# Kernel optimization log

Hardware: AMD Instinct MI355X
Metric: run time of the kernel (lower is better)

## Reference

```python
import jax, jax.numpy as jnp
import numpy as np

HIDDEN = 32
INPUT = 1
OUTPUT = 1


def setup_inputs() -> dict:
    key = jax.random.key(0)
    ks = jax.random.split(key, 7)
    B, T = 4096, 512
    s_ih = 1.0 / np.sqrt(HIDDEN)
    x = jax.random.normal(ks[0], (B, T, INPUT), dtype=jnp.float32)
    # PyTorch LSTM params, gate order i, f, g, o
    W_ih = jax.random.uniform(ks[1], (4 * HIDDEN, INPUT), jnp.float32, -s_ih, s_ih)
    W_hh = jax.random.uniform(ks[2], (4 * HIDDEN, HIDDEN), jnp.float32, -s_ih, s_ih)
    b_ih = jax.random.uniform(ks[3], (4 * HIDDEN,), jnp.float32, -s_ih, s_ih)
    b_hh = jax.random.uniform(ks[4], (4 * HIDDEN,), jnp.float32, -s_ih, s_ih)
    W_fc = jax.random.uniform(ks[5], (OUTPUT, HIDDEN), jnp.float32, -s_ih, s_ih)
    b_fc = jax.random.uniform(ks[6], (OUTPUT,), jnp.float32, -s_ih, s_ih)
    return {"x": x, "W_ih": W_ih, "W_hh": W_hh, "b_ih": b_ih,
            "b_hh": b_hh, "W_fc": W_fc, "b_fc": b_fc}


def _lstm_last_h(x, W_ih, W_hh, b_ih, b_hh):
    B = x.shape[0]
    H = W_hh.shape[1]
    # precompute input contribution for all timesteps: [T, B, 4H]
    xg = jnp.einsum('bti,gi->tbg', x, W_ih) + (b_ih + b_hh)

    def step(carry, xg_t):
        h, c = carry
        gates = xg_t + h @ W_hh.T  # [B, 4H]
        i, f, g, o = jnp.split(gates, 4, axis=-1)
        i = jax.nn.sigmoid(i)
        f = jax.nn.sigmoid(f)
        g = jnp.tanh(g)
        o = jax.nn.sigmoid(o)
        c = f * c + i * g
        h = o * jnp.tanh(c)
        return (h, c), None

    h0 = jnp.zeros((B, H), x.dtype)
    c0 = jnp.zeros((B, H), x.dtype)
    (hT, _), _ = jax.lax.scan(step, (h0, c0), xg)
    return hT  # last timestep hidden state [B, H]


def reference(x, W_ih, W_hh, b_ih, b_hh, W_fc, b_fc):
    hT = _lstm_last_h(x, W_ih, W_hh, b_ih, b_hh)
    return hT @ W_fc.T + b_fc  # [B, OUTPUT]
```

## Files before the change

kernel.cpp:

```cpp
#include <hip/hip_runtime.h>


#define HID 32
#define TSTEPS 512
#define BPW 2
#define BLOCK 64

__device__ __forceinline__ float rcp_fast(float x) {
    return __builtin_amdgcn_rcpf(x);
}
__device__ __forceinline__ float sigmoid_fast(float x) {
    return rcp_fast(1.0f + __expf(-x));
}
__device__ __forceinline__ float tanh_fast(float x) {
    return fmaf(2.0f, rcp_fast(1.0f + __expf(-2.0f * x)), -1.0f);
}

__global__ __launch_bounds__(BLOCK)
__attribute__((amdgpu_waves_per_eu(2, 2)))
void lstm_fused_kernel(const float* __restrict__ x,
                       const float* __restrict__ W_ih,
                       const float* __restrict__ W_hh,
                       const float* __restrict__ b_ih,
                       const float* __restrict__ b_hh,
                       const float* __restrict__ W_fc,
                       const float* __restrict__ b_fc,
                       float* __restrict__ out)
{
    __shared__ __align__(16) float x_s[BPW * TSTEPS];
    __shared__ __align__(16) float h_s[BPW][HID];

    const int tid = threadIdx.x;
    const int lb  = tid >> 5;
    const int j   = tid & 31;
    const int b0  = blockIdx.x * BPW;

    {
        const float4* xsrc = reinterpret_cast<const float4*>(x + (size_t)b0 * TSTEPS);
        float4* xdst = reinterpret_cast<float4*>(x_s);
        #pragma unroll
        for (int k = 0; k < (BPW * TSTEPS) / (4 * BLOCK); ++k)
            xdst[tid + k * BLOCK] = xsrc[tid + k * BLOCK];
    }

    float w0[HID], w1[HID], w2[HID], w3[HID];
    {
        const float4* r0 = reinterpret_cast<const float4*>(W_hh + (size_t)(0 * HID + j) * HID);
        const float4* r1 = reinterpret_cast<const float4*>(W_hh + (size_t)(1 * HID + j) * HID);
        const float4* r2 = reinterpret_cast<const float4*>(W_hh + (size_t)(2 * HID + j) * HID);
        const float4* r3 = reinterpret_cast<const float4*>(W_hh + (size_t)(3 * HID + j) * HID);
        #pragma unroll
        for (int k = 0; k < HID / 4; ++k) {
            float4 v;
            v = r0[k]; w0[4*k]=v.x; w0[4*k+1]=v.y; w0[4*k+2]=v.z; w0[4*k+3]=v.w;
            v = r1[k]; w1[4*k]=v.x; w1[4*k+1]=v.y; w1[4*k+2]=v.z; w1[4*k+3]=v.w;
            v = r2[k]; w2[4*k]=v.x; w2[4*k+1]=v.y; w2[4*k+2]=v.z; w2[4*k+3]=v.w;
            v = r3[k]; w3[4*k]=v.x; w3[4*k+1]=v.y; w3[4*k+2]=v.z; w3[4*k+3]=v.w;
        }
    }
    const float wih0 = W_ih[j],           wih1 = W_ih[HID + j];
    const float wih2 = W_ih[2*HID + j],   wih3 = W_ih[3*HID + j];
    const float bs0  = b_ih[j]           + b_hh[j];
    const float bs1  = b_ih[HID + j]     + b_hh[HID + j];
    const float bs2  = b_ih[2*HID + j]   + b_hh[2*HID + j];
    const float bs3  = b_ih[3*HID + j]   + b_hh[3*HID + j];

    h_s[lb][j] = 0.0f;
    float c = 0.0f;
    float hcur = 0.0f;
    __syncthreads();

    #pragma unroll 1
    for (int t = 0; t < TSTEPS; ++t) {
        const float xv = x_s[lb * TSTEPS + t];

        float a0 = fmaf(xv, wih0, bs0);
        float a1 = fmaf(xv, wih1, bs1);
        float a2 = fmaf(xv, wih2, bs2);
        float a3 = fmaf(xv, wih3, bs3);

        const float4* hr = reinterpret_cast<const float4*>(&h_s[lb][0]);
        #pragma unroll
        for (int k = 0; k < HID / 4; ++k) {
            float4 hv = hr[k];
            a0 = fmaf(hv.x, w0[4*k  ], a0);
            a1 = fmaf(hv.x, w1[4*k  ], a1);
            a2 = fmaf(hv.x, w2[4*k  ], a2);
            a3 = fmaf(hv.x, w3[4*k  ], a3);
            a0 = fmaf(hv.y, w0[4*k+1], a0);
            a1 = fmaf(hv.y, w1[4*k+1], a1);
            a2 = fmaf(hv.y, w2[4*k+1], a2);
            a3 = fmaf(hv.y, w3[4*k+1], a3);
            a0 = fmaf(hv.z, w0[4*k+2], a0);
            a1 = fmaf(hv.z, w1[4*k+2], a1);
            a2 = fmaf(hv.z, w2[4*k+2], a2);
            a3 = fmaf(hv.z, w3[4*k+2], a3);
            a0 = fmaf(hv.w, w0[4*k+3], a0);
            a1 = fmaf(hv.w, w1[4*k+3], a1);
            a2 = fmaf(hv.w, w2[4*k+3], a2);
            a3 = fmaf(hv.w, w3[4*k+3], a3);
        }

        const float ig = sigmoid_fast(a0);
        const float fg = sigmoid_fast(a1);
        const float gg = tanh_fast(a2);
        const float og = sigmoid_fast(a3);
        c    = fmaf(fg, c, ig * gg);
        hcur = og * tanh_fast(c);

        h_s[lb][j] = hcur;
        asm volatile("" ::: "memory");
    }

    float p = hcur * W_fc[j];
    #pragma unroll
    for (int off = 16; off >= 1; off >>= 1)
        p += __shfl_xor(p, off);
    if (j == 0)
        out[b0 + lb] = p + b_fc[0];
}

extern "C" void kernel_launch(void* const* d_in, const int* in_sizes, int n_in,
                              void* d_out, int out_size, void* d_ws, size_t ws_size,
                              hipStream_t stream) {
    const float* x    = (const float*)d_in[0];
    const float* W_ih = (const float*)d_in[1];
    const float* W_hh = (const float*)d_in[2];
    const float* b_ih = (const float*)d_in[3];
    const float* b_hh = (const float*)d_in[4];
    const float* W_fc = (const float*)d_in[5];
    const float* b_fc = (const float*)d_in[6];
    float* out = (float*)d_out;

    const int B = in_sizes[0] / TSTEPS;
    const int grid = B / BPW;
    lstm_fused_kernel<<<grid, BLOCK, 0, stream>>>(x, W_ih, W_hh, b_ih, b_hh,
                                                  W_fc, b_fc, out);
}
```

Measured before the change: 277.1 us.

## Use packed FP32 FMA for recurrent matvec and fold log2e into weights

Stores the W_hh rows as float2 pairs and replaces the scalar FMA chain with v_pk_fma_f32, splitting each gate accumulator into two lanes that are summed at the end. The log2(e) factor, and 2·log2(e) for the tanh gate, is folded into the recurrent weights, input weights and biases, so the activations can call exp2 directly without a multiply. The waves_per_eu attribute is replaced by launch_bounds(64,2). Packed FMA halves the VALU instruction count of the inner product and shortens each serial accumulation chain. The exchange is an extra horizontal add per gate, possible register or packing overhead, and slightly different rounding.

Result: slower. 305.1 us (+10.1%).

```diff
diff --git a/kernel.cpp b/kernel.cpp
--- a/kernel.cpp
+++ b/kernel.cpp
@@ -5,19 +5,27 @@
 #define TSTEPS 512
 #define BPW 2
 #define BLOCK 64
+#define L2E 1.44269504088896340736f
 
+__device__ __forceinline__ float2 pk_fma(float2 a, float2 b, float2 c) {
+    float2 d;
+    asm("v_pk_fma_f32 %0, %1, %2, %3" : "=v"(d) : "v"(a), "v"(b), "v"(c));
+    return d;
+}
 __device__ __forceinline__ float rcp_fast(float x) {
     return __builtin_amdgcn_rcpf(x);
 }
-__device__ __forceinline__ float sigmoid_fast(float x) {
-    return rcp_fast(1.0f + __expf(-x));
+__device__ __forceinline__ float exp2_fast(float x) {
+    return __builtin_amdgcn_exp2f(x);
 }
-__device__ __forceinline__ float tanh_fast(float x) {
-    return fmaf(2.0f, rcp_fast(1.0f + __expf(-2.0f * x)), -1.0f);
+__device__ __forceinline__ float sigmoid_l2(float a) {
+    return rcp_fast(1.0f + exp2_fast(-a));
+}
+__device__ __forceinline__ float tanh_l2(float a) {
+    return fmaf(2.0f, rcp_fast(1.0f + exp2_fast(-a)), -1.0f);
 }
 
-__global__ __launch_bounds__(BLOCK)
-__attribute__((amdgpu_waves_per_eu(2, 2)))
+__global__ __launch_bounds__(BLOCK, 2)
 void lstm_fused_kernel(const float* __restrict__ x,
                        const float* __restrict__ W_ih,
                        const float* __restrict__ W_hh,
@@ -43,7 +51,7 @@
             xdst[tid + k * BLOCK] = xsrc[tid + k * BLOCK];
     }
 
-    float w0[HID], w1[HID], w2[HID], w3[HID];
+    float2 w0[HID/2], w1[HID/2], w2[HID/2], w3[HID/2];
     {
         const float4* r0 = reinterpret_cast<const float4*>(W_hh + (size_t)(0 * HID + j) * HID);
         const float4* r1 = reinterpret_cast<const float4*>(W_hh + (size_t)(1 * HID + j) * HID);
@@ -52,18 +60,24 @@
         #pragma unroll
         for (int k = 0; k < HID / 4; ++k) {
             float4 v;
-            v = r0[k]; w0[4*k]=v.x; w0[4*k+1]=v.y; w0[4*k+2]=v.z; w0[4*k+3]=v.w;
-            v = r1[k]; w1[4*k]=v.x; w1[4*k+1]=v.y; w1[4*k+2]=v.z; w1[4*k+3]=v.w;
-            v = r2[k]; w2[4*k]=v.x; w2[4*k+1]=v.y; w2[4*k+2]=v.z; w2[4*k+3]=v.w;
-            v = r3[k]; w3[4*k]=v.x; w3[4*k+1]=v.y; w3[4*k+2]=v.z; w3[4*k+3]=v.w;
+            v = r0[k]; w0[2*k] = make_float2(v.x*L2E, v.y*L2E);
+                       w0[2*k+1] = make_float2(v.z*L2E, v.w*L2E);
+            v = r1[k]; w1[2*k] = make_float2(v.x*L2E, v.y*L2E);
+                       w1[2*k+1] = make_float2(v.z*L2E, v.w*L2E);
+            v = r2[k]; w2[2*k] = make_float2(v.x*2.0f*L2E, v.y*2.0f*L2E);
+                       w2[2*k+1] = make_float2(v.z*2.0f*L2E, v.w*2.0f*L2E);
+            v = r3[k]; w3[2*k] = make_float2(v.x*L2E, v.y*L2E);
+                       w3[2*k+1] = make_float2(v.z*L2E, v.w*L2E);
         }
     }
-    const float wih0 = W_ih[j],           wih1 = W_ih[HID + j];
-    const float wih2 = W_ih[2*HID + j],   wih3 = W_ih[3*HID + j];
-    const float bs0  = b_ih[j]           + b_hh[j];
-    const float bs1  = b_ih[HID + j]     + b_hh[HID + j];
-    const float bs2  = b_ih[2*HID + j]   + b_hh[2*HID + j];
-    const float bs3  = b_ih[3*HID + j]   + b_hh[3*HID + j];
+    const float wih0 = W_ih[j]         * L2E;
+    const float wih1 = W_ih[HID + j]   * L2E;
+    const float wih2 = W_ih[2*HID + j] * 2.0f * L2E;
+    const float wih3 = W_ih[3*HID + j] * L2E;
+    const float bs0  = (b_ih[j]         + b_hh[j])         * L2E;
+    const float bs1  = (b_ih[HID + j]   + b_hh[HID + j])   * L2E;
+    const float bs2  = (b_ih[2*HID + j] + b_hh[2*HID + j]) * 2.0f * L2E;
+    const float bs3  = (b_ih[3*HID + j] + b_hh[3*HID + j]) * L2E;
 
     h_s[lb][j] = 0.0f;
     float c = 0.0f;
@@ -74,39 +88,37 @@
     for (int t = 0; t < TSTEPS; ++t) {
         const float xv = x_s[lb * TSTEPS + t];
 
-        float a0 = fmaf(xv, wih0, bs0);
-        float a1 = fmaf(xv, wih1, bs1);
-        float a2 = fmaf(xv, wih2, bs2);
-        float a3 = fmaf(xv, wih3, bs3);
+        float2 acc0 = make_float2(fmaf(xv, wih0, bs0), 0.0f);
+        float2 acc1 = make_float2(fmaf(xv, wih1, bs1), 0.0f);
+        float2 acc2 = make_float2(fmaf(xv, wih2, bs2), 0.0f);
+        float2 acc3 = make_float2(fmaf(xv, wih3, bs3), 0.0f);
 
         const float4* hr = reinterpret_cast<const float4*>(&h_s[lb][0]);
         #pragma unroll
         for (int k = 0; k < HID / 4; ++k) {
             float4 hv = hr[k];
-            a0 = fmaf(hv.x, w0[4*k  ], a0);
-            a1 = fmaf(hv.x, w1[4*k  ], a1);
-            a2 = fmaf(hv.x, w2[4*k  ], a2);
-            a3 = fmaf(hv.x, w3[4*k  ], a3);
-            a0 = fmaf(hv.y, w0[4*k+1], a0);
-            a1 = fmaf(hv.y, w1[4*k+1], a1);
-            a2 = fmaf(hv.y, w2[4*k+1], a2);
-            a3 = fmaf(hv.y, w3[4*k+1], a3);
-            a0 = fmaf(hv.z, w0[4*k+2], a0);
-            a1 = fmaf(hv.z, w1[4*k+2], a1);
-            a2 = fmaf(hv.z, w2[4*k+2], a2);
-            a3 = fmaf(hv.z, w3[4*k+2], a3);
-            a0 = fmaf(hv.w, w0[4*k+3], a0);
-            a1 = fmaf(hv.w, w1[4*k+3], a1);
-            a2 = fmaf(hv.w, w2[4*k+3], a2);
-            a3 = fmaf(hv.w, w3[4*k+3], a3);
+            float2 hA = make_float2(hv.x, hv.y);
+            float2 hB = make_float2(hv.z, hv.w);
+            acc0 = pk_fma(hA, w0[2*k], acc0);
+            acc1 = pk_fma(hA, w1[2*k], acc1);
+            acc2 = pk_fma(hA, w2[2*k], acc2);
+            acc3 = pk_fma(hA, w3[2*k], acc3);
+            acc0 = pk_fma(hB, w0[2*k+1], acc0);
+            acc1 = pk_fma(hB, w1[2*k+1], acc1);
+            acc2 = pk_fma(hB, w2[2*k+1], acc2);
+            acc3 = pk_fma(hB, w3[2*k+1], acc3);
         }
+        const float a0 = acc0.x + acc0.y;
+        const float a1 = acc1.x + acc1.y;
+        const float a2 = acc2.x + acc2.y;
+        const float a3 = acc3.x + acc3.y;
 
-        const float ig = sigmoid_fast(a0);
-        const float fg = sigmoid_fast(a1);
-        const float gg = tanh_fast(a2);
-        const float og = sigmoid_fast(a3);
+        const float ig = sigmoid_l2(a0);
+        const float fg = sigmoid_l2(a1);
+        const float gg = tanh_l2(a2);
+        const float og = sigmoid_l2(a3);
         c    = fmaf(fg, c, ig * gg);
-        hcur = og * tanh_fast(c);
+        hcur = og * tanh_l2((2.0f * L2E) * c);
 
         h_s[lb][j] = hcur;
         asm volatile("" ::: "memory");
```

## Hand-write the LSTM recurrence loop in inline GCN assembly

Applied to the files above, without the earlier changes.

Replaces the compiler-generated time loop with a single inline-asm block. W_hh rows are held in fixed VGPRs, h is read from LDS with b128 reads and waitcnt is placed by hand, followed by 128 v_fmac ops and an explicit exp/rcp gate sequence. The aim is to avoid compiler spills and poor scheduling with 128 live weights and to shorten the per-step serial chain. It hardcodes register numbers and relies on wave lockstep for LDS ordering with no barrier, so correctness and portability are fragile.

After: 277.6 us. About the same (+0.2%).

```diff
diff --git a/kernel.cpp b/kernel.cpp
--- a/kernel.cpp
+++ b/kernel.cpp
@@ -1,4 +1,5 @@
 #include <hip/hip_runtime.h>
+#include <stdint.h>
 
 
 #define HID 32
@@ -6,15 +7,11 @@
 #define BPW 2
 #define BLOCK 64
 
-__device__ __forceinline__ float rcp_fast(float x) {
-    return __builtin_amdgcn_rcpf(x);
-}
-__device__ __forceinline__ float sigmoid_fast(float x) {
-    return rcp_fast(1.0f + __expf(-x));
-}
-__device__ __forceinline__ float tanh_fast(float x) {
-    return fmaf(2.0f, rcp_fast(1.0f + __expf(-2.0f * x)), -1.0f);
-}
+#define FMA4(h,wi,wf,wg,wo) \
+  "v_fmac_f32 v192, v" h ", v" wi "\n\t" \
+  "v_fmac_f32 v193, v" h ", v" wf "\n\t" \
+  "v_fmac_f32 v194, v" h ", v" wg "\n\t" \
+  "v_fmac_f32 v195, v" h ", v" wo "\n\t"
 
 __global__ __launch_bounds__(BLOCK)
 __attribute__((amdgpu_waves_per_eu(2, 2)))
@@ -43,74 +40,180 @@
             xdst[tid + k * BLOCK] = xsrc[tid + k * BLOCK];
     }
 
-    float w0[HID], w1[HID], w2[HID], w3[HID];
-    {
-        const float4* r0 = reinterpret_cast<const float4*>(W_hh + (size_t)(0 * HID + j) * HID);
-        const float4* r1 = reinterpret_cast<const float4*>(W_hh + (size_t)(1 * HID + j) * HID);
-        const float4* r2 = reinterpret_cast<const float4*>(W_hh + (size_t)(2 * HID + j) * HID);
-        const float4* r3 = reinterpret_cast<const float4*>(W_hh + (size_t)(3 * HID + j) * HID);
-        #pragma unroll
-        for (int k = 0; k < HID / 4; ++k) {
-            float4 v;
-            v = r0[k]; w0[4*k]=v.x; w0[4*k+1]=v.y; w0[4*k+2]=v.z; w0[4*k+3]=v.w;
-            v = r1[k]; w1[4*k]=v.x; w1[4*k+1]=v.y; w1[4*k+2]=v.z; w1[4*k+3]=v.w;
-            v = r2[k]; w2[4*k]=v.x; w2[4*k+1]=v.y; w2[4*k+2]=v.z; w2[4*k+3]=v.w;
-            v = r3[k]; w3[4*k]=v.x; w3[4*k+1]=v.y; w3[4*k+2]=v.z; w3[4*k+3]=v.w;
-        }
-    }
-    const float wih0 = W_ih[j],           wih1 = W_ih[HID + j];
-    const float wih2 = W_ih[2*HID + j],   wih3 = W_ih[3*HID + j];
+    const uint64_t wa = (uint64_t)(uintptr_t)(W_hh + (size_t)j * HID);
+    const uint32_t wlo = (uint32_t)wa;
+    const uint32_t whi = (uint32_t)(wa >> 32);
+
+    const float wih0 = W_ih[j];
+    const float wih1 = W_ih[HID + j];
+    const float wih2 = W_ih[2 * HID + j];
+    const float wih3 = W_ih[3 * HID + j];
     const float bs0  = b_ih[j]           + b_hh[j];
     const float bs1  = b_ih[HID + j]     + b_hh[HID + j];
-    const float bs2  = b_ih[2*HID + j]   + b_hh[2*HID + j];
-    const float bs3  = b_ih[3*HID + j]   + b_hh[3*HID + j];
-
-    h_s[lb][j] = 0.0f;
-    float c = 0.0f;
-    float hcur = 0.0f;
-    __syncthreads();
-
-    #pragma unroll 1
-    for (int t = 0; t < TSTEPS; ++t) {
-        const float xv = x_s[lb * TSTEPS + t];
-
-        float a0 = fmaf(xv, wih0, bs0);
-        float a1 = fmaf(xv, wih1, bs1);
-        float a2 = fmaf(xv, wih2, bs2);
-        float a3 = fmaf(xv, wih3, bs3);
-
-        const float4* hr = reinterpret_cast<const float4*>(&h_s[lb][0]);
-        #pragma unroll
-        for (int k = 0; k < HID / 4; ++k) {
-            float4 hv = hr[k];
-            a0 = fmaf(hv.x, w0[4*k  ], a0);
-            a1 = fmaf(hv.x, w1[4*k  ], a1);
-            a2 = fmaf(hv.x, w2[4*k  ], a2);
-            a3 = fmaf(hv.x, w3[4*k  ], a3);
-            a0 = fmaf(hv.y, w0[4*k+1], a0);
-            a1 = fmaf(hv.y, w1[4*k+1], a1);
-            a2 = fmaf(hv.y, w2[4*k+1], a2);
-            a3 = fmaf(hv.y, w3[4*k+1], a3);
-            a0 = fmaf(hv.z, w0[4*k+2], a0);
-            a1 = fmaf(hv.z, w1[4*k+2], a1);
-            a2 = fmaf(hv.z, w2[4*k+2], a2);
-            a3 = fmaf(hv.z, w3[4*k+2], a3);
-            a0 = fmaf(hv.w, w0[4*k+3], a0);
-            a1 = fmaf(hv.w, w1[4*k+3], a1);
-            a2 = fmaf(hv.w, w2[4*k+3], a2);
-            a3 = fmaf(hv.w, w3[4*k+3], a3);
-        }
-
-        const float ig = sigmoid_fast(a0);
-        const float fg = sigmoid_fast(a1);
-        const float gg = tanh_fast(a2);
-        const float og = sigmoid_fast(a3);
-        c    = fmaf(fg, c, ig * gg);
-        hcur = og * tanh_fast(c);
-
-        h_s[lb][j] = hcur;
-        asm volatile("" ::: "memory");
-    }
+    const float bs2  = b_ih[2 * HID + j] + b_hh[2 * HID + j];
+    const float bs3  = b_ih[3 * HID + j] + b_hh[3 * HID + j];
+
+    const uint32_t xb = (uint32_t)(uintptr_t)(&x_s[0]) + (uint32_t)(lb * TSTEPS * 4);
+    const uint32_t hr = (uint32_t)(uintptr_t)(&h_s[0][0]) + (uint32_t)(lb * HID * 4);
+    const uint32_t hw = hr + (uint32_t)(j * 4);
+
+    asm volatile(
+        "v_mov_b32 v208, %[wlo]\n\t"
+        "v_mov_b32 v209, %[whi]\n\t"
+        "global_load_dwordx4 v[64:67],   v[208:209], off\n\t"
+        "global_load_dwordx4 v[68:71],   v[208:209], off offset:16\n\t"
+        "global_load_dwordx4 v[72:75],   v[208:209], off offset:32\n\t"
+        "global_load_dwordx4 v[76:79],   v[208:209], off offset:48\n\t"
+        "global_load_dwordx4 v[80:83],   v[208:209], off offset:64\n\t"
+        "global_load_dwordx4 v[84:87],   v[208:209], off offset:80\n\t"
+        "global_load_dwordx4 v[88:91],   v[208:209], off offset:96\n\t"
+        "global_load_dwordx4 v[92:95],   v[208:209], off offset:112\n\t"
+        "v_add_co_u32 v208, vcc, 0x1000, v208\n\t"
+        "v_addc_co_u32 v209, vcc, 0, v209, vcc\n\t"
+        "global_load_dwordx4 v[96:99],   v[208:209], off\n\t"
+        "global_load_dwordx4 v[100:103], v[208:209], off offset:16\n\t"
+        "global_load_dwordx4 v[104:107], v[208:209], off offset:32\n\t"
+        "global_load_dwordx4 v[108:111], v[208:209], off offset:48\n\t"
+        "global_load_dwordx4 v[112:115], v[208:209], off offset:64\n\t"
+        "global_load_dwordx4 v[116:119], v[208:209], off offset:80\n\t"
+        "global_load_dwordx4 v[120:123], v[208:209], off offset:96\n\t"
+        "global_load_dwordx4 v[124:127], v[208:209], off offset:112\n\t"
+        "v_add_co_u32 v208, vcc, 0x1000, v208\n\t"
+        "v_addc_co_u32 v209, vcc, 0, v209, vcc\n\t"
+        "global_load_dwordx4 v[128:131], v[208:209], off\n\t"
+        "global_load_dwordx4 v[132:135], v[208:209], off offset:16\n\t"
+        "global_load_dwordx4 v[136:139], v[208:209], off offset:32\n\t"
+        "global_load_dwordx4 v[140:143], v[208:209], off offset:48\n\t"
+        "global_load_dwordx4 v[144:147], v[208:209], off offset:64\n\t"
+        "global_load_dwordx4 v[148:151], v[208:209], off offset:80\n\t"
+        "global_load_dwordx4 v[152:155], v[208:209], off offset:96\n\t"
+        "global_load_dwordx4 v[156:159], v[208:209], off offset:112\n\t"
+        "v_add_co_u32 v208, vcc, 0x1000, v208\n\t"
+        "v_addc_co_u32 v209, vcc, 0, v209, vcc\n\t"
+        "global_load_dwordx4 v[160:163], v[208:209], off\n\t"
+        "global_load_dwordx4 v[164:167], v[208:209], off offset:16\n\t"
+        "global_load_dwordx4 v[168:171], v[208:209], off offset:32\n\t"
+        "global_load_dwordx4 v[172:175], v[208:209], off offset:48\n\t"
+        "global_load_dwordx4 v[176:179], v[208:209], off offset:64\n\t"
+        "global_load_dwordx4 v[180:183], v[208:209], off offset:80\n\t"
+        "global_load_dwordx4 v[184:187], v[208:209], off offset:96\n\t"
+        "global_load_dwordx4 v[188:191], v[208:209], off offset:112\n\t"
+        "v_mov_b32 v205, 0\n\t"
+        "v_mov_b32 v206, 0\n\t"
+        "ds_write_b32 %[hw], v206\n\t"
+        "v_mov_b32 v207, %[xb]\n\t"
+        "v_mov_b32 v210, 0\n\t"
+        "s_waitcnt vmcnt(0)\n\t"
+        "LSTM_T_%=:\n\t"
+        "ds_read_b32 v196, v207\n\t"
+        "ds_read_b128 v[32:35], %[hr]\n\t"
+        "ds_read_b128 v[36:39], %[hr] offset:16\n\t"
+        "ds_read_b128 v[40:43], %[hr] offset:32\n\t"
+        "ds_read_b128 v[44:47], %[hr] offset:48\n\t"
+        "ds_read_b128 v[48:51], %[hr] offset:64\n\t"
+        "ds_read_b128 v[52:55], %[hr] offset:80\n\t"
+        "ds_read_b128 v[56:59], %[hr] offset:96\n\t"
+        "ds_read_b128 v[60:63], %[hr] offset:112\n\t"
+        "v_add_u32 v207, 4, v207\n\t"
+        "s_waitcnt lgkmcnt(8)\n\t"
+        "v_fma_f32 v192, v196, %[wi0], %[q0]\n\t"
+        "v_fma_f32 v193, v196, %[wi1], %[q1]\n\t"
+        "v_fma_f32 v194, v196, %[wi2], %[q2]\n\t"
+        "v_fma_f32 v195, v196, %[wi3], %[q3]\n\t"
+        "s_waitcnt lgkmcnt(0)\n\t"
+        FMA4("32","64","96","128","160")
+        FMA4("33","65","97","129","161")
+        FMA4("34","66","98","130","162")
+        FMA4("35","67","99","131","163")
+        FMA4("36","68","100","132","164")
+        FMA4("37","69","101","133","165")
+        FMA4("38","70","102","134","166")
+        FMA4("39","71","103","135","167")
+        FMA4("40","72","104","136","168")
+        FMA4("41","73","105","137","169")
+        FMA4("42","74","106","138","170")
+        FMA4("43","75","107","139","171")
+        FMA4("44","76","108","140","172")
+        FMA4("45","77","109","141","173")
+        FMA4("46","78","110","142","174")
+        FMA4("47","79","111","143","175")
+        FMA4("48","80","112","144","176")
+        FMA4("49","81","113","145","177")
+        FMA4("50","82","114","146","178")
+        FMA4("51","83","115","147","179")
+        FMA4("52","84","116","148","180")
+        FMA4("53","85","117","149","181")
+        FMA4("54","86","118","150","182")
+        FMA4("55","87","119","151","183")
+        FMA4("56","88","120","152","184")
+        FMA4("57","89","121","153","185")
+        FMA4("58","90","122","154","186")
+        FMA4("59","91","123","155","187")
+        FMA4("60","92","124","156","188")
+        FMA4("61","93","125","157","189")
+        FMA4("62","94","126","158","190")
+        FMA4("63","95","127","159","191")
+        "v_mul_f32 v197, 0xbfb8aa3b, v192\n\t"
+        "v_mul_f32 v198, 0xbfb8aa3b, v193\n\t"
+        "v_mul_f32 v199, 0xc038aa3b, v194\n\t"
+        "v_mul_f32 v200, 0xbfb8aa3b, v195\n\t"
+        "v_exp_f32 v197, v197\n\t"
+        "v_exp_f32 v198, v198\n\t"
+        "v_exp_f32 v199, v199\n\t"
+        "v_exp_f32 v200, v200\n\t"
+        "v_add_f32 v197, 1.0, v197\n\t"
+        "v_add_f32 v198, 1.0, v198\n\t"
+        "v_add_f32 v199, 1.0, v199\n\t"
+        "v_add_f32 v200, 1.0, v200\n\t"
+        "v_rcp_f32 v197, v197\n\t"
+        "v_rcp_f32 v198, v198\n\t"
+        "v_rcp_f32 v199, v199\n\t"
+        "v_rcp_f32 v200, v200\n\t"
+        "v_fma_f32 v201, 2.0, v199, -1.0\n\t"
+        "v_mul_f32 v202, v197, v201\n\t"
+        "v_fma_f32 v205, v198, v205, v202\n\t"
+        "v_mul_f32 v203, 0xc038aa3b, v205\n\t"
+        "v_exp_f32 v203, v203\n\t"
+        "v_add_u32 v210, 1, v210\n\t"
+        "v_add_f32 v203, 1.0, v203\n\t"
+        "v_rcp_f32 v203, v203\n\t"
+        "v_cmp_gt_u32 vcc, 512, v210\n\t"
+        "v_fma_f32 v204, 2.0, v203, -1.0\n\t"
+        "v_mul_f32 v206, v200, v204\n\t"
+        "ds_write_b32 %[hw], v206\n\t"
+        "s_cbranch_vccnz LSTM_T_%=\n\t"
+        "s_waitcnt vmcnt(0) lgkmcnt(0)\n\t"
+        :
+        : [wlo] "v"(wlo), [whi] "v"(whi),
+          [xb] "v"(xb), [hr] "v"(hr), [hw] "v"(hw),
+          [wi0] "v"(wih0), [wi1] "v"(wih1), [wi2] "v"(wih2), [wi3] "v"(wih3),
+          [q0] "v"(bs0), [q1] "v"(bs1), [q2] "v"(bs2), [q3] "v"(bs3)
+        : "memory", "vcc",
+          "v32","v33","v34","v35","v36","v37","v38","v39",
+          "v40","v41","v42","v43","v44","v45","v46","v47",
+          "v48","v49","v50","v51","v52","v53","v54","v55",
+          "v56","v57","v58","v59","v60","v61","v62","v63",
+          "v64","v65","v66","v67","v68","v69","v70","v71",
+          "v72","v73","v74","v75","v76","v77","v78","v79",
+          "v80","v81","v82","v83","v84","v85","v86","v87",
+          "v88","v89","v90","v91","v92","v93","v94","v95",
+          "v96","v97","v98","v99","v100","v101","v102","v103",
+          "v104","v105","v106","v107","v108","v109","v110","v111",
+          "v112","v113","v114","v115","v116","v117","v118","v119",
+          "v120","v121","v122","v123","v124","v125","v126","v127",
+          "v128","v129","v130","v131","v132","v133","v134","v135",
+          "v136","v137","v138","v139","v140","v141","v142","v143",
+          "v144","v145","v146","v147","v148","v149","v150","v151",
+          "v152","v153","v154","v155","v156","v157","v158","v159",
+          "v160","v161","v162","v163","v164","v165","v166","v167",
+          "v168","v169","v170","v171","v172","v173","v174","v175",
+          "v176","v177","v178","v179","v180","v181","v182","v183",
+          "v184","v185","v186","v187","v188","v189","v190","v191",
+          "v192","v193","v194","v195","v196","v197","v198","v199",
+          "v200","v201","v202","v203","v204","v205","v206","v207",
+          "v208","v209","v210");
+
+    const float hcur = h_s[lb][j];
 
     float p = hcur * W_fc[j];
     #pragma unroll
```
